# Optimization experiments

Measured on AMD Instinct MI355X. Metric: run time of the kernel, lower is better.

The kernel has to match this reference:

```python
import jax, jax.numpy as jnp
import numpy as np

WS = (7, 7)   # window size
SS = (3, 3)   # shift size
NH = 3        # num heads
EPS = 1e-5


def _rel_index():
    # relative position index [N, N], computed exactly as in WindowAttention.__init__
    coords = np.stack(np.meshgrid(np.arange(WS[0]), np.arange(WS[1]), indexing='ij'))  # [2,7,7]
    cf = coords.reshape(2, -1)                     # [2, N]
    rel = (cf[:, :, None] - cf[:, None, :]).transpose(1, 2, 0)  # [N, N, 2]
    rel[..., 0] += WS[0] - 1
    rel[..., 1] += WS[1] - 1
    idx = rel[..., 0] * (2 * WS[1] - 1) + rel[..., 1]
    return jnp.asarray(idx)


def _attn_mask(H, W):
    # standard Swin shifted-window mask: [nW, N, N] of {0, -100}
    img = np.zeros((H, W), dtype=np.float32)
    cnt = 0
    for hs in (slice(0, -WS[0]), slice(-WS[0], -SS[0]), slice(-SS[0], None)):
        for ws_ in (slice(0, -WS[1]), slice(-WS[1], -SS[1]), slice(-SS[1], None)):
            img[hs, ws_] = cnt
            cnt += 1
    mw = img.reshape(H // WS[0], WS[0], W // WS[1], WS[1]).transpose(0, 2, 1, 3)
    mw = mw.reshape(-1, WS[0] * WS[1])            # [nW, N]
    am = mw[:, None, :] - mw[:, :, None]
    am = np.where(am != 0, np.float32(-100.0), np.float32(0.0))
    return jnp.asarray(am)


def _ln(x, g, b):
    m = x.mean(-1, keepdims=True)
    v = ((x - m) ** 2).mean(-1, keepdims=True)
    return (x - m) * jax.lax.rsqrt(v + EPS) * g + b


def _forward(x, norm1_g, norm1_b, qkv_w, qkv_b, rel_table, proj_w, proj_b,
             norm2_g, norm2_b, mlp_w1, mlp_b1, mlp_w2, mlp_b2):
    B, C, H, W = x.shape
    N = WS[0] * WS[1]
    hd = C // NH
    scale = hd ** -0.5

    # norm1 over channels (token layout [B, HW, C])
    xt = x.reshape(B, C, H * W).transpose(0, 2, 1)
    xn = _ln(xt, norm1_g, norm1_b).transpose(0, 2, 1).reshape(B, C, H, W)

    # cyclic shift + window partition -> [B*nW, N, C]
    shifted = jnp.roll(xn, (-SS[0], -SS[1]), axis=(2, 3))
    nWh, nWw = H // WS[0], W // WS[1]
    xw = shifted.transpose(0, 2, 3, 1)  # [B, H, W, C]
    xwin = xw.reshape(B, nWh, WS[0], nWw, WS[1], C).transpose(0, 1, 3, 2, 4, 5)
    xwin = xwin.reshape(-1, N, C)

    # windowed attention with relative position bias + shift mask
    qkv = (xwin @ qkv_w.T + qkv_b).reshape(-1, N, 3, NH, hd).transpose(2, 0, 3, 1, 4)
    q, k, v = qkv[0] * scale, qkv[1], qkv[2]            # [B_, h, N, hd]
    attn = jnp.einsum('bhnd,bhmd->bhnm', q, k)          # [B_, h, N, N]
    bias = rel_table[_rel_index()]                       # [N, N, h]
    attn = attn + bias.transpose(2, 0, 1)[None]
    mask = _attn_mask(H, W)                              # [nW, N, N]
    nW = mask.shape[0]
    attn = attn.reshape(-1, nW, NH, N, N) + mask[None, :, None]
    attn = jax.nn.softmax(attn.reshape(-1, NH, N, N), axis=-1)
    out = jnp.einsum('bhnm,bhmd->bhnd', attn, v).transpose(0, 2, 1, 3).reshape(-1, N, C)
    out = out @ proj_w.T + proj_b

    # window reverse + reverse shift -> [B, C, H, W]
    xr = out.reshape(B, nWh, nWw, WS[0], WS[1], C).transpose(0, 1, 3, 2, 4, 5)
    xr = xr.reshape(B, H, W, C).transpose(0, 3, 1, 2)
    xr = jnp.roll(xr, (SS[0], SS[1]), axis=(2, 3))

    x = x + xr  # residual (drop_path = Identity)

    # MLP branch with pre-norm over channels
    xt = x.reshape(B, C, H * W).transpose(0, 2, 1)
    h = _ln(xt, norm2_g, norm2_b)
    h = jax.nn.gelu(h @ mlp_w1.T + mlp_b1, approximate=False)
    h = h @ mlp_w2.T + mlp_b2
    return x + h.transpose(0, 2, 1).reshape(B, C, H, W)


def setup_inputs() -> dict:
    key = jax.random.key(0)
    ks = jax.random.split(key, 8)
    B, C, H, W = 8, 96, 224, 224
    hid = 384
    s = 0.02
    return {
        'x': jax.random.normal(ks[0], (B, C, H, W), jnp.float32),
        'norm1_g': jnp.ones((C,), jnp.float32),
        'norm1_b': jnp.zeros((C,), jnp.float32),
        'qkv_w': jax.random.normal(ks[1], (3 * C, C), jnp.float32) * s,
        'qkv_b': jnp.zeros((3 * C,), jnp.float32),
        'rel_table': jax.random.normal(ks[2], (169, NH), jnp.float32) * s,
        'proj_w': jax.random.normal(ks[3], (C, C), jnp.float32) * s,
        'proj_b': jnp.zeros((C,), jnp.float32),
        'norm2_g': jnp.ones((C,), jnp.float32),
        'norm2_b': jnp.zeros((C,), jnp.float32),
        'mlp_w1': jax.random.normal(ks[4], (hid, C), jnp.float32) * s,
        'mlp_b1': jnp.zeros((hid,), jnp.float32),
        'mlp_w2': jax.random.normal(ks[5], (C, hid), jnp.float32) * s,
        'mlp_b2': jnp.zeros((C,), jnp.float32),
    }


def reference(x, norm1_g, norm1_b, qkv_w, qkv_b, rel_table, proj_w, proj_b,
              norm2_g, norm2_b, mlp_w1, mlp_b1, mlp_w2, mlp_b2):
    return _forward(x, norm1_g, norm1_b, qkv_w, qkv_b, rel_table, proj_w, proj_b,
                    norm2_g, norm2_b, mlp_w1, mlp_b1, mlp_w2, mlp_b2)
```

## Files before the change

### kernel.cpp

```cpp
#include <hip/hip_runtime.h>
#include <hip/hip_bf16.h>

typedef __attribute__((ext_vector_type(8))) short short8;
typedef __attribute__((ext_vector_type(4))) short s16x4;
typedef __attribute__((ext_vector_type(4))) float f32x4;

#define D_H   224
#define D_W   224
#define D_HW  50176
#define SCALE 0.17677669529663687f

#define WO_QKVW  0
#define WO_PROJW 27648
#define WO_W1    36864
#define WO_W2    73728
#define WO_TOT   110592

#define XT_SH 0
#define YT_SH 38535168
#define W_SH  77070336
#define TAB_SH (W_SH + WO_TOT)
#define WS_NEED ((size_t)(77070336 + 110592) * 2 + 65536)

static __device__ __forceinline__ short f2s(float v) {
    union { __hip_bfloat16 b; short s; } u; u.b = __float2bfloat16(v); return u.s;
}
static __device__ __forceinline__ float s2f(short s) {
    union { short s; __hip_bfloat16 b; } u; u.s = s; return __bfloat162float(u.b);
}

#define MFMA(a, b, c) __builtin_amdgcn_mfma_f32_16x16x32_bf16((a), (b), (c), 0, 0, 0)

static __device__ __forceinline__ short8 normfrag(const short* p, const float* g,
                                                  const float* b, int c0, float m, float rs) {
    short8 r = *(const short8*)p;
    short8 o;
#pragma unroll
    for (int j = 0; j < 8; j++) o[j] = f2s((s2f(r[j]) - m) * rs * g[c0 + j] + b[c0 + j]);
    return o;
}

static __device__ __forceinline__ float erf_fast(float x) {
    float a = fabsf(x);
    float t = __builtin_amdgcn_rcpf(1.f + 0.3275911f * a);
    float p = t * (0.254829592f + t * (-0.284496736f + t * (1.421413741f +
              t * (-1.453152027f + t * 1.061405429f))));
    float y = 1.f - p * __expf(-a * a);
    return copysignf(y, x);
}

__global__ __launch_bounds__(256) void k_prep(
    const float* __restrict__ qkvw, const float* __restrict__ projw,
    const float* __restrict__ w1, const float* __restrict__ w2,
    const float* __restrict__ relt, short* __restrict__ ws, float* __restrict__ tabf)
{
    const int bid = blockIdx.x;
    if (bid < 108) {
        int i4 = bid * 256 + threadIdx.x;
        const float* src; int off;
        if (i4 < 6912)        { src = qkvw;  off = 0; }
        else if (i4 < 9216)   { src = projw; off = 6912; }
        else if (i4 < 18432)  { src = w1;    off = 9216; }
        else                  { src = w2;    off = 18432; }
        f32x4 v = *(const f32x4*)&src[(i4 - off) * 4];
        s16x4 s;
#pragma unroll
        for (int j = 0; j < 4; j++) s[j] = f2s(v[j]);
        *(s16x4*)&ws[i4 * 4] = s;
    } else {
        int i = (bid - 108) * 256 + threadIdx.x;
        int n = i >> 6, m = i & 63;
        int nn = (n < 49) ? n : 48;
        int mm = (m < 49) ? m : 48;
        int r1 = nn / 7, c1 = nn - r1 * 7;
        int r2 = mm / 7, c2 = mm - r2 * 7;
        int ri = ((r1 - r2 + 6) * 13 + (c1 - c2 + 6)) * 3;
        f32x4 o = { relt[ri + 0], relt[ri + 1], relt[ri + 2], 0.f };
        *(f32x4*)&tabf[i * 4] = o;
    }
}

__global__ __launch_bounds__(256) void k_t(const float* __restrict__ x, short* __restrict__ xt)
{
    __shared__ short tile[224][128];
    const int tid = threadIdx.x;
    const int bh = blockIdx.x;
    const int b = bh / 224, h = bh - b * 224;
    const int pbase = (b * 96) * D_HW + h * 224;

#pragma unroll
    for (int k = 0; k < 6; k++) {
        int idx = tid + k * 256;
        if (idx < 1344) {
            int c4 = idx / 56, w4 = idx - c4 * 56;
            float vv[4][4];
#pragma unroll
            for (int j = 0; j < 4; j++) {
                f32x4 v = *(const f32x4*)&x[pbase + (c4 * 4 + j) * D_HW + w4 * 4];
#pragma unroll
                for (int i = 0; i < 4; i++) vv[j][i] = v[i];
            }
#pragma unroll
            for (int i = 0; i < 4; i++) {
                int w = w4 * 4 + i;
                s16x4 o;
#pragma unroll
                for (int j = 0; j < 4; j++) o[j] = f2s(vv[j][i]);
                *(s16x4*)&tile[w][(c4 ^ (w & 31)) * 4] = o;
            }
        }
    }
    __syncthreads();
    const int obase = ((b * 224 + h) * 224) * 96;
#pragma unroll
    for (int k = 0; k < 11; k++) {
        int idx = tid + k * 256;
        if (idx < 2688) {
            int w = idx / 12, s = idx - w * 12;
            int kk = w & 31;
            s16x4 a = *(const s16x4*)&tile[w][((2 * s) ^ kk) * 4];
            s16x4 c = *(const s16x4*)&tile[w][((2 * s + 1) ^ kk) * 4];
            short8 o;
            o[0] = a[0]; o[1] = a[1]; o[2] = a[2]; o[3] = a[3];
            o[4] = c[0]; o[5] = c[1]; o[6] = c[2]; o[7] = c[3];
            *(short8*)&xt[obase + w * 96 + s * 8] = o;
        }
    }
}

__global__ __launch_bounds__(256, 3) void k_attn_t(
    const short* __restrict__ xt, const float* __restrict__ n1g, const float* __restrict__ n1b,
    const float* __restrict__ qkvb, const float* __restrict__ tabf,
    const float* __restrict__ projb, const short* __restrict__ wsw, short* __restrict__ yt)
{
    __shared__ short qk[64][200];
    __shared__ __align__(16) short region[11520];
    short (*xs)[104] = (short(*)[104])region;
    short (*ps)[72]  = (short(*)[72])region;
    short (*vt)[72]  = (short(*)[72])(region + 4608);
    __shared__ int   cnt_s[64];
    __shared__ float mean_s[64], rstd_s[64];

    const int tid  = threadIdx.x;
    const int wave = tid >> 6, lane = tid & 63;
    const int l16  = lane & 15, q8 = (lane >> 4) * 8, q4 = (lane >> 4) * 4;
    const int t0   = wave * 16;

    const short* qkvw_bf  = wsw + WO_QKVW;
    const short* projw_bf = wsw + WO_PROJW;

    const int wi = blockIdx.x;
    const int b  = wi >> 10, nw = wi & 1023;
    const int wh = nw >> 5, ww = nw & 31;
    const bool edge = (wh == 31) || (ww == 31);

    if (tid < 64) {
        int t = (tid < 49) ? tid : 48;
        int r = t / 7, c = t - r * 7;
        int sh = wh * 7 + r, sw = ww * 7 + c;
        int rh = (sh < 217) ? 0 : ((sh < 221) ? 1 : 2);
        int rw = (sw < 217) ? 0 : ((sw < 221) ? 1 : 2);
        cnt_s[tid] = rh * 3 + rw;
    }
#pragma unroll
    for (int k = 0; k < 3; k++) {
        int idx = tid + k * 256;
        int t = idx / 12, s = idx - t * 12;
        short8 v = {0, 0, 0, 0, 0, 0, 0, 0};
        if (t < 49) {
            int r = t / 7, cc = t - r * 7;
            int hh = wh * 7 + r + 3;  if (hh >= D_H) hh -= D_H;
            int w2 = ww * 7 + cc + 3; if (w2 >= D_W) w2 -= D_W;
            v = *(const short8*)&xt[((b * 224 + hh) * 224 + w2) * 96 + s * 8];
        }
        *(short8*)&xs[t][s * 8] = v;
    }
    __syncthreads();

    {
        int t = tid >> 2, p = tid & 3;
        float s = 0.f, s2 = 0.f;
#pragma unroll
        for (int i = 0; i < 6; i++) {
            s16x4 v4 = *(const s16x4*)&xs[t][p * 24 + i * 4];
#pragma unroll
            for (int j = 0; j < 4; j++) { float v = s2f(v4[j]); s += v; s2 += v * v; }
        }
        s += __shfl_xor(s, 1); s2 += __shfl_xor(s2, 1);
        s += __shfl_xor(s, 2); s2 += __shfl_xor(s2, 2);
        if (p == 0) {
            float m = s * (1.f / 96.f);
            float var = s2 * (1.f / 96.f) - m * m;
            mean_s[t] = m; rstd_s[t] = rsqrtf(var + 1e-5f);
        }
    }

    const float m0 = mean_s[t0 + l16], rs0 = rstd_s[t0 + l16];
    short8 a0 = normfrag(&xs[t0 + l16][q8],      n1g, n1b, q8,      m0, rs0);
    short8 a1 = normfrag(&xs[t0 + l16][32 + q8], n1g, n1b, 32 + q8, m0, rs0);
    short8 a2 = normfrag(&xs[t0 + l16][64 + q8], n1g, n1b, 64 + q8, m0, rs0);

    short8 wA0, wA1, wA2, wB0, wB1, wB2;
    {
        const short* w = qkvw_bf + l16 * 96;
        wA0 = *(const short8*)&w[q8];
        wA1 = *(const short8*)&w[32 + q8];
        wA2 = *(const short8*)&w[64 + q8];
    }
    __syncthreads();

#pragma unroll
    for (int g = 0; g < 18; g++) {
        const int jc = g / 6, nt = g - jc * 6;
        const int jj = nt * 16 + l16;
        if (g < 17) {
            int g2 = g + 1, jc2 = g2 / 6, nt2 = g2 - jc2 * 6;
            const short* w = qkvw_bf + (jc2 * 96 + nt2 * 16 + l16) * 96;
            wB0 = *(const short8*)&w[q8];
            wB1 = *(const short8*)&w[32 + q8];
            wB2 = *(const short8*)&w[64 + q8];
        }
        f32x4 acc = {0.f, 0.f, 0.f, 0.f};
        acc = MFMA(a0, wA0, acc);
        acc = MFMA(a1, wA1, acc);
        acc = MFMA(a2, wA2, acc);
        float bias = qkvb[jc * 96 + jj];
        if (jc == 0) {
#pragma unroll
            for (int r = 0; r < 4; r++) qk[t0 + q4 + r][jj] = f2s((acc[r] + bias) * SCALE);
        } else if (jc == 1) {
#pragma unroll
            for (int r = 0; r < 4; r++) qk[t0 + q4 + r][96 + jj] = f2s(acc[r] + bias);
        } else {
            s16x4 v4;
#pragma unroll
            for (int r = 0; r < 4; r++) v4[r] = f2s(acc[r] + bias);
            *(s16x4*)&vt[jj][t0 + q4] = v4;
        }
        wA0 = wB0; wA1 = wB1; wA2 = wB2;
    }

    float biasv[4][4][3];
#pragma unroll
    for (int nt = 0; nt < 4; nt++) {
        int m  = nt * 16 + l16;
        int cm = cnt_s[m];
#pragma unroll
        for (int r = 0; r < 4; r++) {
            int n = t0 + q4 + r;
            f32x4 t4 = *(const f32x4*)&tabf[(n * 64 + m) * 4];
            float mk = (edge && (cnt_s[n] != cm)) ? -100.f : 0.f;
            biasv[nt][r][0] = t4[0] + mk;
            biasv[nt][r][1] = t4[1] + mk;
            biasv[nt][r][2] = t4[2] + mk;
        }
    }
    const bool inval3 = (l16 != 0);

    __syncthreads();

#pragma unroll
    for (int h = 0; h < 3; h++) {
        short8 aq = *(const short8*)&qk[t0 + l16][h * 32 + q8];
        f32x4 sv[4];
#pragma unroll
        for (int nt = 0; nt < 4; nt++) {
            f32x4 z = {0.f, 0.f, 0.f, 0.f};
            sv[nt] = MFMA(aq, *(const short8*)&qk[nt * 16 + l16][96 + h * 32 + q8], z);
        }
        float mx[4] = {-1e30f, -1e30f, -1e30f, -1e30f};
#pragma unroll
        for (int nt = 0; nt < 4; nt++) {
#pragma unroll
            for (int r = 0; r < 4; r++) {
                float v = sv[nt][r] + biasv[nt][r][h];
                if (nt == 3 && inval3) v = -1e30f;
                sv[nt][r] = v;
                mx[r] = fmaxf(mx[r], v);
            }
        }
#pragma unroll
        for (int d = 1; d < 16; d <<= 1) {
#pragma unroll
            for (int r = 0; r < 4; r++) mx[r] = fmaxf(mx[r], __shfl_xor(mx[r], d));
        }
        float sm[4] = {0.f, 0.f, 0.f, 0.f};
#pragma unroll
        for (int nt = 0; nt < 4; nt++) {
#pragma unroll
            for (int r = 0; r < 4; r++) {
                float e = (nt == 3 && inval3) ? 0.f : __expf(sv[nt][r] - mx[r]);
                sv[nt][r] = e;
                sm[r] += e;
            }
        }
#pragma unroll
        for (int d = 1; d < 16; d <<= 1) {
#pragma unroll
            for (int r = 0; r < 4; r++) sm[r] += __shfl_xor(sm[r], d);
        }
        float inv[4];
#pragma unroll
        for (int r = 0; r < 4; r++) inv[r] = __builtin_amdgcn_rcpf(sm[r]);
#pragma unroll
        for (int nt = 0; nt < 4; nt++) {
#pragma unroll
            for (int r = 0; r < 4; r++)
                ps[t0 + q4 + r][nt * 16 + l16] = f2s(sv[nt][r] * inv[r]);
        }
        short8 p0 = *(const short8*)&ps[t0 + l16][q8];
        short8 p1 = *(const short8*)&ps[t0 + l16][32 + q8];
#pragma unroll
        for (int nt = 0; nt < 2; nt++) {
            f32x4 acc = {0.f, 0.f, 0.f, 0.f};
            acc = MFMA(p0, *(const short8*)&vt[h * 32 + nt * 16 + l16][q8],      acc);
            acc = MFMA(p1, *(const short8*)&vt[h * 32 + nt * 16 + l16][32 + q8], acc);
            int d = nt * 16 + l16;
#pragma unroll
            for (int r = 0; r < 4; r++) {
                int t = t0 + q4 + r;
                if (t < 49) qk[t][h * 32 + d] = f2s(acc[r]);
            }
        }
    }

    {
        const short* w = projw_bf + l16 * 96;
        wA0 = *(const short8*)&w[q8];
        wA1 = *(const short8*)&w[32 + q8];
        wA2 = *(const short8*)&w[64 + q8];
    }
    short8 o0 = *(const short8*)&qk[t0 + l16][q8];
    short8 o1 = *(const short8*)&qk[t0 + l16][32 + q8];
    short8 o2 = *(const short8*)&qk[t0 + l16][64 + q8];
#pragma unroll
    for (int nt = 0; nt < 6; nt++) {
        int i = nt * 16 + l16;
        if (nt < 5) {
            const short* w = projw_bf + ((nt + 1) * 16 + l16) * 96;
            wB0 = *(const short8*)&w[q8];
            wB1 = *(const short8*)&w[32 + q8];
            wB2 = *(const short8*)&w[64 + q8];
        }
        f32x4 acc = {0.f, 0.f, 0.f, 0.f};
        acc = MFMA(o0, wA0, acc);
        acc = MFMA(o1, wA1, acc);
        acc = MFMA(o2, wA2, acc);
        float pb = projb[i];
#pragma unroll
        for (int r = 0; r < 4; r++) {
            int t = t0 + q4 + r;
            if (t < 49) qk[t][i] = f2s(acc[r] + pb);
        }
        wA0 = wB0; wA1 = wB1; wA2 = wB2;
    }
    __syncthreads();
#pragma unroll
    for (int k = 0; k < 3; k++) {
        int idx = tid + k * 256;
        if (idx < 588) {
            int t = idx / 12, s = idx - t * 12;
            int r = t / 7, cc = t - r * 7;
            int hh = wh * 7 + r + 3;  if (hh >= D_H) hh -= D_H;
            int w2 = ww * 7 + cc + 3; if (w2 >= D_W) w2 -= D_W;
            *(short8*)&yt[((b * 224 + hh) * 224 + w2) * 96 + s * 8] =
                *(const short8*)&qk[t][s * 8];
        }
    }
}

#define XCOL(row, c) ((((((c) >> 3) ^ (((row) >> 2) & 7)) << 3)) | ((c) & 7))

__global__ __launch_bounds__(256, 3) void k_mlp_t(
    const float* __restrict__ x, const short* __restrict__ ytk, float* __restrict__ y,
    const float* __restrict__ n2g, const float* __restrict__ n2b,
    const float* __restrict__ b1, const float* __restrict__ b2, const short* __restrict__ wsw)
{
    __shared__ __align__(16) char region[96 * 104 * 2];
    short (*xs)[128] = (short(*)[128])region;
    short (*wb)[104] = (short(*)[104])region;
    __shared__ __align__(16) short hb[64][104];
    __shared__ float mean_s[64], rstd_s[64];

    const int tid  = threadIdx.x;
    const int wave = tid >> 6, lane = tid & 63;
    const int l16  = lane & 15, q8 = (lane >> 4) * 8, q4 = (lane >> 4) * 4;
    const int t0   = wave * 16;

    const short* w1_bf = wsw + WO_W1;
    const short* w2_bf = wsw + WO_W2;

    const int T0 = blockIdx.x * 64;
    const int b  = T0 / D_HW;
    const int p0 = T0 - b * D_HW;
    const int base = (b * 96) * D_HW + p0;

#pragma unroll
    for (int k = 0; k < 3; k++) {
        int idx = tid + k * 256;
        int t = idx / 12, s = idx - t * 12;
        *(short8*)&xs[t][(s ^ ((t >> 2) & 7)) << 3] =
            *(const short8*)&ytk[(T0 + t) * 96 + s * 8];
    }
    __syncthreads();

    float yv[6][4];
#pragma unroll
    for (int k = 0; k < 6; k++) {
        int idx = tid + k * 256;
        int c = idx >> 4, q = idx & 15;
        f32x4 xv = *(const f32x4*)&x[base + c * D_HW + q * 4];
        int ch = ((c >> 3) ^ (q & 7)) * 8 + (c & 7);
#pragma unroll
        for (int j = 0; j < 4; j++) {
            float v = xv[j] + s2f(xs[q * 4 + j][ch]);
            yv[k][j] = v;
            xs[q * 4 + j][ch] = f2s(v);
        }
    }
    __syncthreads();

    {
        int t = tid >> 2, p = tid & 3;
        float s = 0.f, s2 = 0.f;
#pragma unroll
        for (int i = 0; i < 6; i++) {
            int c = p * 24 + i * 4;
            s16x4 v4 = *(const s16x4*)&xs[t][XCOL(t, c)];
#pragma unroll
            for (int j = 0; j < 4; j++) { float v = s2f(v4[j]); s += v; s2 += v * v; }
        }
        s += __shfl_xor(s, 1); s2 += __shfl_xor(s2, 1);
        s += __shfl_xor(s, 2); s2 += __shfl_xor(s2, 2);
        if (p == 0) {
            float m = s * (1.f / 96.f);
            float var = s2 * (1.f / 96.f) - m * m;
            mean_s[t] = m; rstd_s[t] = rsqrtf(var + 1e-5f);
        }
    }

    short8 xa[3];
    {
        int t = t0 + l16;
        float m = mean_s[t], rs = rstd_s[t];
        int key = (t >> 2) & 7;
#pragma unroll
        for (int kk = 0; kk < 3; kk++) {
            int ch = kk * 4 + (lane >> 4);
            xa[kk] = normfrag(&xs[t][(ch ^ key) << 3], n2g, n2b, ch * 8, m, rs);
        }
    }

    f32x4 c2[6];
#pragma unroll
    for (int nt = 0; nt < 6; nt++) c2[nt] = (f32x4){0.f, 0.f, 0.f, 0.f};

    short8 pf[5];
#pragma unroll
    for (int k = 0; k < 5; k++) {
        int idx = tid + k * 256; if (idx > 1151) idx = 1151;
        pf[k] = *(const short8*)&w1_bf[idx * 8];
    }
#pragma unroll
    for (int jc = 0; jc < 4; jc++) {
        __syncthreads();
#pragma unroll
        for (int k = 0; k < 5; k++) {
            int idx = tid + k * 256;
            if (idx < 1152) { int j = idx / 12, s = idx - j * 12; *(short8*)&wb[j][s * 8] = pf[k]; }
        }
        __syncthreads();
#pragma unroll
        for (int k = 0; k < 5; k++) {
            int idx = tid + k * 256; if (idx > 1151) idx = 1151;
            int o = idx / 12, s = idx - o * 12;
            pf[k] = *(const short8*)&w2_bf[o * 384 + jc * 96 + s * 8];
        }
#pragma unroll
        for (int nt = 0; nt < 6; nt++) {
            int jj = nt * 16 + l16;
            f32x4 acc = {0.f, 0.f, 0.f, 0.f};
            acc = MFMA(xa[0], *(const short8*)&wb[jj][q8],      acc);
            acc = MFMA(xa[1], *(const short8*)&wb[jj][32 + q8], acc);
            acc = MFMA(xa[2], *(const short8*)&wb[jj][64 + q8], acc);
            float bb = b1[jc * 96 + jj];
#pragma unroll
            for (int r = 0; r < 4; r++) {
                float v = acc[r] + bb;
                float g = 0.5f * v * (1.f + erf_fast(v * 0.7071067811865475f));
                hb[t0 + q4 + r][jj] = f2s(g);
            }
        }
        __syncthreads();
#pragma unroll
        for (int k = 0; k < 5; k++) {
            int idx = tid + k * 256;
            if (idx < 1152) { int j = idx / 12, s = idx - j * 12; *(short8*)&wb[j][s * 8] = pf[k]; }
        }
        __syncthreads();
        if (jc < 3) {
#pragma unroll
            for (int k = 0; k < 5; k++) {
                int idx = tid + k * 256; if (idx > 1151) idx = 1151;
                pf[k] = *(const short8*)&w1_bf[(jc + 1) * 9216 + idx * 8];
            }
        }
        {
            short8 h0 = *(const short8*)&hb[t0 + l16][q8];
            short8 h1 = *(const short8*)&hb[t0 + l16][32 + q8];
            short8 h2 = *(const short8*)&hb[t0 + l16][64 + q8];
#pragma unroll
            for (int nt = 0; nt < 6; nt++) {
                int jj = nt * 16 + l16;
                c2[nt] = MFMA(h0, *(const short8*)&wb[jj][q8],      c2[nt]);
                c2[nt] = MFMA(h1, *(const short8*)&wb[jj][32 + q8], c2[nt]);
                c2[nt] = MFMA(h2, *(const short8*)&wb[jj][64 + q8], c2[nt]);
            }
        }
    }
    __syncthreads();

#pragma unroll
    for (int nt = 0; nt < 6; nt++) {
        int i = nt * 16 + l16;
        float bo = b2[i];
#pragma unroll
        for (int r = 0; r < 4; r++) {
            int t = t0 + q4 + r;
            xs[t][XCOL(t, i)] = f2s(bo + c2[nt][r]);
        }
    }
    __syncthreads();
#pragma unroll
    for (int k = 0; k < 6; k++) {
        int idx = tid + k * 256;
        int c = idx >> 4, q = idx & 15;
        int ch = ((c >> 3) ^ (q & 7)) * 8 + (c & 7);
        f32x4 o;
#pragma unroll
        for (int j = 0; j < 4; j++) o[j] = yv[k][j] + s2f(xs[q * 4 + j][ch]);
        *(f32x4*)&y[base + c * D_HW + q * 4] = o;
    }
}

__global__ __launch_bounds__(256, 3) void k_attn_f(
    const float* __restrict__ x, const float* __restrict__ n1g, const float* __restrict__ n1b,
    const float* __restrict__ qkvb, const float* __restrict__ relt,
    const float* __restrict__ projb, const short* __restrict__ wsw, float* __restrict__ y)
{
    __shared__ short qk[64][200];
    __shared__ short vt[96][72];
    __shared__ __align__(16) short xs[64][104];
    short (*ps)[72] = (short(*)[72])xs;
    __shared__ int   cnt_s[64];
    __shared__ float mean_s[64], rstd_s[64];

    const int tid  = threadIdx.x;
    const int wave = tid >> 6, lane = tid & 63;
    const int l16  = lane & 15, q8 = (lane >> 4) * 8, q4 = (lane >> 4) * 4;
    const int t0   = wave * 16;

    const short* qkvw_bf  = wsw + WO_QKVW;
    const short* projw_bf = wsw + WO_PROJW;

    const int wi = blockIdx.x;
    const int b  = wi >> 10, nw = wi & 1023;
    const int wh = nw >> 5, ww = nw & 31;
    const bool edge = (wh == 31) || (ww == 31);

    if (tid < 64) {
        int t = (tid < 49) ? tid : 48;
        int r = t / 7, c = t - r * 7;
        int sh = wh * 7 + r, sw = ww * 7 + c;
        int rh = (sh < 217) ? 0 : ((sh < 221) ? 1 : 2);
        int rw = (sw < 217) ? 0 : ((sw < 221) ? 1 : 2);
        cnt_s[tid] = rh * 3 + rw;
    }
    {
        int t = lane;
        int r = t / 7, cc = t - r * 7;
        int hh = wh * 7 + r + 3;  if (hh >= D_H) hh -= D_H;
        int w2 = ww * 7 + cc + 3; if (w2 >= D_W) w2 -= D_W;
        int off0 = (b * 96) * D_HW + hh * D_W + w2;
#pragma unroll
        for (int n = 0; n < 6; n++) {
            int c0 = wave * 24 + n * 4;
            s16x4 v4 = {0, 0, 0, 0};
            if (t < 49) {
                v4[0] = f2s(x[off0 + (c0 + 0) * D_HW]);
                v4[1] = f2s(x[off0 + (c0 + 1) * D_HW]);
                v4[2] = f2s(x[off0 + (c0 + 2) * D_HW]);
                v4[3] = f2s(x[off0 + (c0 + 3) * D_HW]);
            }
            *(s16x4*)&xs[t][c0] = v4;
        }
    }
    __syncthreads();
    {
        int t = tid >> 2, p = tid & 3;
        float s = 0.f, s2 = 0.f;
#pragma unroll
        for (int i = 0; i < 6; i++) {
            s16x4 v4 = *(const s16x4*)&xs[t][p * 24 + i * 4];
#pragma unroll
            for (int j = 0; j < 4; j++) { float v = s2f(v4[j]); s += v; s2 += v * v; }
        }
        s += __shfl_xor(s, 1); s2 += __shfl_xor(s2, 1);
        s += __shfl_xor(s, 2); s2 += __shfl_xor(s2, 2);
        if (p == 0) {
            float m = s * (1.f / 96.f);
            float var = s2 * (1.f / 96.f) - m * m;
            mean_s[t] = m; rstd_s[t] = rsqrtf(var + 1e-5f);
        }
    }
    __syncthreads();

    const float m0 = mean_s[t0 + l16], rs0 = rstd_s[t0 + l16];
    short8 a0 = normfrag(&xs[t0 + l16][q8],      n1g, n1b, q8,      m0, rs0);
    short8 a1 = normfrag(&xs[t0 + l16][32 + q8], n1g, n1b, 32 + q8, m0, rs0);
    short8 a2 = normfrag(&xs[t0 + l16][64 + q8], n1g, n1b, 64 + q8, m0, rs0);

#pragma unroll
    for (int jc = 0; jc < 3; jc++) {
#pragma unroll
        for (int nt = 0; nt < 6; nt++) {
            int jj = nt * 16 + l16;
            const short* wr = qkvw_bf + (jc * 96 + jj) * 96;
            f32x4 acc = {0.f, 0.f, 0.f, 0.f};
            acc = MFMA(a0, *(const short8*)&wr[q8],      acc);
            acc = MFMA(a1, *(const short8*)&wr[32 + q8], acc);
            acc = MFMA(a2, *(const short8*)&wr[64 + q8], acc);
            float bias = qkvb[jc * 96 + jj];
            if (jc == 0) {
#pragma unroll
                for (int r = 0; r < 4; r++) qk[t0 + q4 + r][jj] = f2s((acc[r] + bias) * SCALE);
            } else if (jc == 1) {
#pragma unroll
                for (int r = 0; r < 4; r++) qk[t0 + q4 + r][96 + jj] = f2s(acc[r] + bias);
            } else {
                s16x4 v4;
#pragma unroll
                for (int r = 0; r < 4; r++) v4[r] = f2s(acc[r] + bias);
                *(s16x4*)&vt[jj][t0 + q4] = v4;
            }
        }
    }

    float biasv[4][4][3];
#pragma unroll
    for (int nt = 0; nt < 4; nt++) {
        int m  = nt * 16 + l16;
        int mm = (m < 49) ? m : 48;
        int r2 = mm / 7, c2 = mm - r2 * 7;
        int cm = cnt_s[m];
#pragma unroll
        for (int r = 0; r < 4; r++) {
            int n  = t0 + q4 + r;
            int nn = (n < 49) ? n : 48;
            int r1 = nn / 7, c1 = nn - r1 * 7;
            int ri = ((r1 - r2 + 6) * 13 + (c1 - c2 + 6)) * 3;
            float mk = (edge && (cnt_s[n] != cm)) ? -100.f : 0.f;
            biasv[nt][r][0] = relt[ri + 0] + mk;
            biasv[nt][r][1] = relt[ri + 1] + mk;
            biasv[nt][r][2] = relt[ri + 2] + mk;
        }
    }
    const bool inval3 = (l16 != 0);

#pragma unroll
    for (int h = 0; h < 3; h++) {
        __syncthreads();
        short8 aq = *(const short8*)&qk[t0 + l16][h * 32 + q8];
        f32x4 sv[4];
#pragma unroll
        for (int nt = 0; nt < 4; nt++) {
            f32x4 z = {0.f, 0.f, 0.f, 0.f};
            sv[nt] = MFMA(aq, *(const short8*)&qk[nt * 16 + l16][96 + h * 32 + q8], z);
        }
        float mx[4] = {-1e30f, -1e30f, -1e30f, -1e30f};
#pragma unroll
        for (int nt = 0; nt < 4; nt++) {
#pragma unroll
            for (int r = 0; r < 4; r++) {
                float v = sv[nt][r] + biasv[nt][r][h];
                if (nt == 3 && inval3) v = -1e30f;
                sv[nt][r] = v;
                mx[r] = fmaxf(mx[r], v);
            }
        }
#pragma unroll
        for (int d = 1; d < 16; d <<= 1) {
#pragma unroll
            for (int r = 0; r < 4; r++) mx[r] = fmaxf(mx[r], __shfl_xor(mx[r], d));
        }
        float sm[4] = {0.f, 0.f, 0.f, 0.f};
#pragma unroll
        for (int nt = 0; nt < 4; nt++) {
#pragma unroll
            for (int r = 0; r < 4; r++) {
                float e = (nt == 3 && inval3) ? 0.f : __expf(sv[nt][r] - mx[r]);
                sv[nt][r] = e;
                sm[r] += e;
            }
        }
#pragma unroll
        for (int d = 1; d < 16; d <<= 1) {
#pragma unroll
            for (int r = 0; r < 4; r++) sm[r] += __shfl_xor(sm[r], d);
        }
        float inv[4];
#pragma unroll
        for (int r = 0; r < 4; r++) inv[r] = 1.f / sm[r];
#pragma unroll
        for (int nt = 0; nt < 4; nt++) {
#pragma unroll
            for (int r = 0; r < 4; r++)
                ps[t0 + q4 + r][nt * 16 + l16] = f2s(sv[nt][r] * inv[r]);
        }
        __syncthreads();
        short8 p0 = *(const short8*)&ps[t0 + l16][q8];
        short8 p1 = *(const short8*)&ps[t0 + l16][32 + q8];
#pragma unroll
        for (int nt = 0; nt < 2; nt++) {
            f32x4 acc = {0.f, 0.f, 0.f, 0.f};
            acc = MFMA(p0, *(const short8*)&vt[h * 32 + nt * 16 + l16][q8],      acc);
            acc = MFMA(p1, *(const short8*)&vt[h * 32 + nt * 16 + l16][32 + q8], acc);
            int d = nt * 16 + l16;
#pragma unroll
            for (int r = 0; r < 4; r++) {
                int t = t0 + q4 + r;
                if (t < 49) qk[t][h * 32 + d] = f2s(acc[r]);
            }
        }
    }

    __syncthreads();
    short8 o0 = *(const short8*)&qk[t0 + l16][q8];
    short8 o1 = *(const short8*)&qk[t0 + l16][32 + q8];
    short8 o2 = *(const short8*)&qk[t0 + l16][64 + q8];
    int  po[4];
    bool tv[4];
#pragma unroll
    for (int r = 0; r < 4; r++) {
        int t = t0 + q4 + r;
        tv[r] = (t < 49);
        int tt = tv[r] ? t : 0;
        int rr = tt / 7, cc = tt - rr * 7;
        int hh = wh * 7 + rr + 3;  if (hh >= D_H) hh -= D_H;
        int w2 = ww * 7 + cc + 3;  if (w2 >= D_W) w2 -= D_W;
        po[r] = (b * 96) * D_HW + hh * D_W + w2;
    }
#pragma unroll
    for (int nt = 0; nt < 6; nt++) {
        int i = nt * 16 + l16;
        const short* wr = projw_bf + i * 96;
        f32x4 acc = {0.f, 0.f, 0.f, 0.f};
        acc = MFMA(o0, *(const short8*)&wr[q8],      acc);
        acc = MFMA(o1, *(const short8*)&wr[32 + q8], acc);
        acc = MFMA(o2, *(const short8*)&wr[64 + q8], acc);
        float pb = projb[i];
#pragma unroll
        for (int r = 0; r < 4; r++) {
            if (tv[r]) {
                int off = po[r] + i * D_HW;
                y[off] = x[off] + acc[r] + pb;
            }
        }
    }
}

__global__ __launch_bounds__(256, 3) void k_mlp_f(
    float* __restrict__ y, const float* __restrict__ n2g, const float* __restrict__ n2b,
    const float* __restrict__ b1, const float* __restrict__ b2, const short* __restrict__ wsw)
{
    __shared__ short xs[128][104];
    __shared__ short hb[128][104];
    __shared__ float mean_s[128], rstd_s[128];

    const int tid  = threadIdx.x;
    const int wave = tid >> 6, lane = tid & 63;
    const int l16  = lane & 15, q8 = (lane >> 4) * 8, q4 = (lane >> 4) * 4;
    const int t0   = wave * 32;

    const short* w1_bf = wsw + WO_W1;
    const short* w2_bf = wsw + WO_W2;

    const int T0 = blockIdx.x * 128;
    const int b  = T0 / D_HW;
    const int p0 = T0 - b * D_HW;
    const int base = (b * 96) * D_HW + p0;

    for (int idx = tid; idx < 96 * 32; idx += 256) {
        int c = idx >> 5, q = idx & 31;
        f32x4 v4 = *(const f32x4*)&y[base + c * D_HW + q * 4];
        xs[q * 4 + 0][c] = f2s(v4[0]);
        xs[q * 4 + 1][c] = f2s(v4[1]);
        xs[q * 4 + 2][c] = f2s(v4[2]);
        xs[q * 4 + 3][c] = f2s(v4[3]);
    }
    __syncthreads();
    {
        int t = tid >> 1, p = tid & 1;
        float s = 0.f, s2 = 0.f;
#pragma unroll
        for (int i = 0; i < 12; i++) {
            s16x4 v4 = *(const s16x4*)&xs[t][p * 48 + i * 4];
#pragma unroll
            for (int j = 0; j < 4; j++) { float v = s2f(v4[j]); s += v; s2 += v * v; }
        }
        s += __shfl_xor(s, 1); s2 += __shfl_xor(s2, 1);
        float m = s * (1.f / 96.f);
        float var = s2 * (1.f / 96.f) - m * m;
        mean_s[t] = m; rstd_s[t] = rsqrtf(var + 1e-5f);
    }
    __syncthreads();

    short8 xa[2][3];
#pragma unroll
    for (int s = 0; s < 2; s++) {
        float m = mean_s[t0 + s * 16 + l16], rs = rstd_s[t0 + s * 16 + l16];
#pragma unroll
        for (int kk = 0; kk < 3; kk++)
            xa[s][kk] = normfrag(&xs[t0 + s * 16 + l16][kk * 32 + q8], n2g, n2b,
                                 kk * 32 + q8, m, rs);
    }

    f32x4 c2[2][6];
#pragma unroll
    for (int s = 0; s < 2; s++)
#pragma unroll
        for (int nt = 0; nt < 6; nt++) c2[s][nt] = (f32x4){0.f, 0.f, 0.f, 0.f};

    for (int jc = 0; jc < 4; jc++) {
#pragma unroll
        for (int s = 0; s < 2; s++) {
#pragma unroll
            for (int nt = 0; nt < 6; nt++) {
                int jj = nt * 16 + l16;
                const short* wr = w1_bf + (jc * 96 + jj) * 96;
                f32x4 acc = {0.f, 0.f, 0.f, 0.f};
                acc = MFMA(xa[s][0], *(const short8*)&wr[q8],      acc);
                acc = MFMA(xa[s][1], *(const short8*)&wr[32 + q8], acc);
                acc = MFMA(xa[s][2], *(const short8*)&wr[64 + q8], acc);
                float bb = b1[jc * 96 + jj];
#pragma unroll
                for (int r = 0; r < 4; r++) {
                    float v = acc[r] + bb;
                    float g = 0.5f * v * (1.f + erf_fast(v * 0.7071067811865475f));
                    hb[t0 + s * 16 + q4 + r][jj] = f2s(g);
                }
            }
        }
        __syncthreads();
#pragma unroll
        for (int s = 0; s < 2; s++) {
            short8 h0 = *(const short8*)&hb[t0 + s * 16 + l16][q8];
            short8 h1 = *(const short8*)&hb[t0 + s * 16 + l16][32 + q8];
            short8 h2 = *(const short8*)&hb[t0 + s * 16 + l16][64 + q8];
#pragma unroll
            for (int nt = 0; nt < 6; nt++) {
                const short* wr = w2_bf + (nt * 16 + l16) * 384 + jc * 96;
                c2[s][nt] = MFMA(h0, *(const short8*)&wr[q8],      c2[s][nt]);
                c2[s][nt] = MFMA(h1, *(const short8*)&wr[32 + q8], c2[s][nt]);
                c2[s][nt] = MFMA(h2, *(const short8*)&wr[64 + q8], c2[s][nt]);
            }
        }
        __syncthreads();
    }

#pragma unroll
    for (int s = 0; s < 2; s++)
#pragma unroll
        for (int nt = 0; nt < 6; nt++) {
            int i = nt * 16 + l16;
            float bo = b2[i];
#pragma unroll
            for (int r = 0; r < 4; r++)
                xs[t0 + s * 16 + q4 + r][i] = f2s(bo + c2[s][nt][r]);
        }
    __syncthreads();
    for (int idx = tid; idx < 96 * 32; idx += 256) {
        int c = idx >> 5, q = idx & 31;
        int off = base + c * D_HW + q * 4;
        f32x4 v4 = *(const f32x4*)&y[off];
        v4[0] += s2f(xs[q * 4 + 0][c]);
        v4[1] += s2f(xs[q * 4 + 1][c]);
        v4[2] += s2f(xs[q * 4 + 2][c]);
        v4[3] += s2f(xs[q * 4 + 3][c]);
        *(f32x4*)&y[off] = v4;
    }
}

extern "C" void kernel_launch(void* const* d_in, const int* in_sizes, int n_in,
                              void* d_out, int out_size, void* d_ws, size_t ws_size,
                              hipStream_t stream) {
    const float* x    = (const float*)d_in[0];
    const float* n1g  = (const float*)d_in[1];
    const float* n1b  = (const float*)d_in[2];
    const float* qkvw = (const float*)d_in[3];
    const float* qkvb = (const float*)d_in[4];
    const float* relt = (const float*)d_in[5];
    const float* projw= (const float*)d_in[6];
    const float* projb= (const float*)d_in[7];
    const float* n2g  = (const float*)d_in[8];
    const float* n2b  = (const float*)d_in[9];
    const float* w1   = (const float*)d_in[10];
    const float* b1   = (const float*)d_in[11];
    const float* w2   = (const float*)d_in[12];
    const float* b2   = (const float*)d_in[13];
    float* y  = (float*)d_out;
    short* ws = (short*)d_ws;

    if (ws_size >= WS_NEED) {
        short* xt  = ws + XT_SH;
        short* ytk = ws + YT_SH;
        short* wbf = ws + W_SH;
        float* tabf = (float*)(ws + TAB_SH);
        k_prep<<<124, 256, 0, stream>>>(qkvw, projw, w1, w2, relt, wbf, tabf);
        k_t<<<1792, 256, 0, stream>>>(x, xt);
        k_attn_t<<<8192, 256, 0, stream>>>(xt, n1g, n1b, qkvb, tabf, projb, wbf, ytk);
        k_mlp_t<<<6272, 256, 0, stream>>>(x, ytk, y, n2g, n2b, b1, b2, wbf);
    } else {
        k_prep<<<108, 256, 0, stream>>>(qkvw, projw, w1, w2, relt, ws, (float*)ws);
        k_attn_f<<<8192, 256, 0, stream>>>(x, n1g, n1b, qkvb, relt, projb, ws, y);
        k_mlp_f<<<3136, 256, 0, stream>>>(y, n2g, n2b, b1, b2, ws);
    }
}
```

Measured before the change: 676.9 us.

## Move LayerNorm1 into transpose kernel and compute rel-pos bias inline

LayerNorm1 statistics and normalization move from the attention kernel into the transpose kernel, so the stored bf16 token tensor is already normalized and the attention kernel loads its A fragments directly. The precomputed relative-position bias table is dropped, and the attention kernel gathers bias values straight from the small rel_table with index arithmetic. This removes per-window LN work and the table build/load, but adds an extra LN pass in the transpose kernel and scattered small loads in attention.

Measured after the change: 632.0 us. 6.6% less time.

```diff
diff --git a/kernel.cpp b/kernel.cpp
--- a/kernel.cpp
+++ b/kernel.cpp
@@ -19,8 +19,7 @@
 #define XT_SH 0
 #define YT_SH 38535168
 #define W_SH  77070336
-#define TAB_SH (W_SH + WO_TOT)
-#define WS_NEED ((size_t)(77070336 + 110592) * 2 + 65536)
+#define WS_NEED ((size_t)(77070336 + 110592) * 2)
 
 static __device__ __forceinline__ short f2s(float v) {
     union { __hip_bfloat16 b; short s; } u; u.b = __float2bfloat16(v); return u.s;
@@ -51,38 +50,27 @@
 
 __global__ __launch_bounds__(256) void k_prep(
     const float* __restrict__ qkvw, const float* __restrict__ projw,
-    const float* __restrict__ w1, const float* __restrict__ w2,
-    const float* __restrict__ relt, short* __restrict__ ws, float* __restrict__ tabf)
+    const float* __restrict__ w1, const float* __restrict__ w2, short* __restrict__ ws)
 {
-    const int bid = blockIdx.x;
-    if (bid < 108) {
-        int i4 = bid * 256 + threadIdx.x;
-        const float* src; int off;
-        if (i4 < 6912)        { src = qkvw;  off = 0; }
-        else if (i4 < 9216)   { src = projw; off = 6912; }
-        else if (i4 < 18432)  { src = w1;    off = 9216; }
-        else                  { src = w2;    off = 18432; }
-        f32x4 v = *(const f32x4*)&src[(i4 - off) * 4];
-        s16x4 s;
-#pragma unroll
-        for (int j = 0; j < 4; j++) s[j] = f2s(v[j]);
-        *(s16x4*)&ws[i4 * 4] = s;
-    } else {
-        int i = (bid - 108) * 256 + threadIdx.x;
-        int n = i >> 6, m = i & 63;
-        int nn = (n < 49) ? n : 48;
-        int mm = (m < 49) ? m : 48;
-        int r1 = nn / 7, c1 = nn - r1 * 7;
-        int r2 = mm / 7, c2 = mm - r2 * 7;
-        int ri = ((r1 - r2 + 6) * 13 + (c1 - c2 + 6)) * 3;
-        f32x4 o = { relt[ri + 0], relt[ri + 1], relt[ri + 2], 0.f };
-        *(f32x4*)&tabf[i * 4] = o;
-    }
-}
-
-__global__ __launch_bounds__(256) void k_t(const float* __restrict__ x, short* __restrict__ xt)
+    int i4 = blockIdx.x * 256 + threadIdx.x;
+    const float* src; int off;
+    if (i4 < 6912)        { src = qkvw;  off = 0; }
+    else if (i4 < 9216)   { src = projw; off = 6912; }
+    else if (i4 < 18432)  { src = w1;    off = 9216; }
+    else                  { src = w2;    off = 18432; }
+    f32x4 v = *(const f32x4*)&src[(i4 - off) * 4];
+    s16x4 s;
+#pragma unroll
+    for (int j = 0; j < 4; j++) s[j] = f2s(v[j]);
+    *(s16x4*)&ws[i4 * 4] = s;
+}
+
+__global__ __launch_bounds__(256) void k_t(
+    const float* __restrict__ x, const float* __restrict__ n1g,
+    const float* __restrict__ n1b, short* __restrict__ xt)
 {
     __shared__ short tile[224][128];
+    __shared__ float mean_s[224], rstd_s[224];
     const int tid = threadIdx.x;
     const int bh = blockIdx.x;
     const int b = bh / 224, h = bh - b * 224;
@@ -111,6 +99,20 @@
         }
     }
     __syncthreads();
+    if (tid < 224) {
+        int key = tid & 31;
+        float s = 0.f, s2 = 0.f;
+#pragma unroll
+        for (int c4 = 0; c4 < 24; c4++) {
+            s16x4 v4 = *(const s16x4*)&tile[tid][(c4 ^ key) << 2];
+#pragma unroll
+            for (int j = 0; j < 4; j++) { float v = s2f(v4[j]); s += v; s2 += v * v; }
+        }
+        float m = s * (1.f / 96.f);
+        float var = s2 * (1.f / 96.f) - m * m;
+        mean_s[tid] = m; rstd_s[tid] = rsqrtf(var + 1e-5f);
+    }
+    __syncthreads();
     const int obase = ((b * 224 + h) * 224) * 96;
 #pragma unroll
     for (int k = 0; k < 11; k++) {
@@ -118,20 +120,27 @@
         if (idx < 2688) {
             int w = idx / 12, s = idx - w * 12;
             int kk = w & 31;
-            s16x4 a = *(const s16x4*)&tile[w][((2 * s) ^ kk) * 4];
-            s16x4 c = *(const s16x4*)&tile[w][((2 * s + 1) ^ kk) * 4];
+            s16x4 a = *(const s16x4*)&tile[w][((2 * s) ^ kk) << 2];
+            s16x4 c = *(const s16x4*)&tile[w][((2 * s + 1) ^ kk) << 2];
+            float m = mean_s[w], rs = rstd_s[w];
+            f32x4 g0 = *(const f32x4*)&n1g[s * 8];
+            f32x4 g1 = *(const f32x4*)&n1g[s * 8 + 4];
+            f32x4 b0 = *(const f32x4*)&n1b[s * 8];
+            f32x4 b1 = *(const f32x4*)&n1b[s * 8 + 4];
             short8 o;
-            o[0] = a[0]; o[1] = a[1]; o[2] = a[2]; o[3] = a[3];
-            o[4] = c[0]; o[5] = c[1]; o[6] = c[2]; o[7] = c[3];
+#pragma unroll
+            for (int j = 0; j < 4; j++) o[j]     = f2s((s2f(a[j]) - m) * rs * g0[j] + b0[j]);
+#pragma unroll
+            for (int j = 0; j < 4; j++) o[4 + j] = f2s((s2f(c[j]) - m) * rs * g1[j] + b1[j]);
             *(short8*)&xt[obase + w * 96 + s * 8] = o;
         }
     }
 }
 
 __global__ __launch_bounds__(256, 3) void k_attn_t(
-    const short* __restrict__ xt, const float* __restrict__ n1g, const float* __restrict__ n1b,
-    const float* __restrict__ qkvb, const float* __restrict__ tabf,
-    const float* __restrict__ projb, const short* __restrict__ wsw, short* __restrict__ yt)
+    const short* __restrict__ xt, const float* __restrict__ qkvb,
+    const float* __restrict__ relt, const float* __restrict__ projb,
+    const short* __restrict__ wsw, short* __restrict__ yt)
 {
     __shared__ short qk[64][200];
     __shared__ __align__(16) short region[11520];
@@ -139,7 +148,6 @@
     short (*ps)[72]  = (short(*)[72])region;
     short (*vt)[72]  = (short(*)[72])(region + 4608);
     __shared__ int   cnt_s[64];
-    __shared__ float mean_s[64], rstd_s[64];
 
     const int tid  = threadIdx.x;
     const int wave = tid >> 6, lane = tid & 63;
@@ -177,28 +185,9 @@
     }
     __syncthreads();
 
-    {
-        int t = tid >> 2, p = tid & 3;
-        float s = 0.f, s2 = 0.f;
-#pragma unroll
-        for (int i = 0; i < 6; i++) {
-            s16x4 v4 = *(const s16x4*)&xs[t][p * 24 + i * 4];
-#pragma unroll
-            for (int j = 0; j < 4; j++) { float v = s2f(v4[j]); s += v; s2 += v * v; }
-        }
-        s += __shfl_xor(s, 1); s2 += __shfl_xor(s2, 1);
-        s += __shfl_xor(s, 2); s2 += __shfl_xor(s2, 2);
-        if (p == 0) {
-            float m = s * (1.f / 96.f);
-            float var = s2 * (1.f / 96.f) - m * m;
-            mean_s[t] = m; rstd_s[t] = rsqrtf(var + 1e-5f);
-        }
-    }
-
-    const float m0 = mean_s[t0 + l16], rs0 = rstd_s[t0 + l16];
-    short8 a0 = normfrag(&xs[t0 + l16][q8],      n1g, n1b, q8,      m0, rs0);
-    short8 a1 = normfrag(&xs[t0 + l16][32 + q8], n1g, n1b, 32 + q8, m0, rs0);
-    short8 a2 = normfrag(&xs[t0 + l16][64 + q8], n1g, n1b, 64 + q8, m0, rs0);
+    short8 a0 = *(const short8*)&xs[t0 + l16][q8];
+    short8 a1 = *(const short8*)&xs[t0 + l16][32 + q8];
+    short8 a2 = *(const short8*)&xs[t0 + l16][64 + q8];
 
     short8 wA0, wA1, wA2, wB0, wB1, wB2;
     {
@@ -244,15 +233,19 @@
 #pragma unroll
     for (int nt = 0; nt < 4; nt++) {
         int m  = nt * 16 + l16;
+        int mm = (m < 49) ? m : 48;
+        int r2 = mm / 7, c2 = mm - r2 * 7;
         int cm = cnt_s[m];
 #pragma unroll
         for (int r = 0; r < 4; r++) {
-            int n = t0 + q4 + r;
-            f32x4 t4 = *(const f32x4*)&tabf[(n * 64 + m) * 4];
+            int n  = t0 + q4 + r;
+            int nn = (n < 49) ? n : 48;
+            int r1 = nn / 7, c1 = nn - r1 * 7;
+            int ri = ((r1 - r2 + 6) * 13 + (c1 - c2 + 6)) * 3;
             float mk = (edge && (cnt_s[n] != cm)) ? -100.f : 0.f;
-            biasv[nt][r][0] = t4[0] + mk;
-            biasv[nt][r][1] = t4[1] + mk;
-            biasv[nt][r][2] = t4[2] + mk;
+            biasv[nt][r][0] = relt[ri + 0] + mk;
+            biasv[nt][r][1] = relt[ri + 1] + mk;
+            biasv[nt][r][2] = relt[ri + 2] + mk;
         }
     }
     const bool inval3 = (l16 != 0);
@@ -915,13 +908,12 @@
         short* xt  = ws + XT_SH;
         short* ytk = ws + YT_SH;
         short* wbf = ws + W_SH;
-        float* tabf = (float*)(ws + TAB_SH);
-        k_prep<<<124, 256, 0, stream>>>(qkvw, projw, w1, w2, relt, wbf, tabf);
-        k_t<<<1792, 256, 0, stream>>>(x, xt);
-        k_attn_t<<<8192, 256, 0, stream>>>(xt, n1g, n1b, qkvb, tabf, projb, wbf, ytk);
+        k_prep<<<108, 256, 0, stream>>>(qkvw, projw, w1, w2, wbf);
+        k_t<<<1792, 256, 0, stream>>>(x, n1g, n1b, xt);
+        k_attn_t<<<8192, 256, 0, stream>>>(xt, qkvb, relt, projb, wbf, ytk);
         k_mlp_t<<<6272, 256, 0, stream>>>(x, ytk, y, n2g, n2b, b1, b2, wbf);
     } else {
-        k_prep<<<108, 256, 0, stream>>>(qkvw, projw, w1, w2, relt, ws, (float*)ws);
+        k_prep<<<108, 256, 0, stream>>>(qkvw, projw, w1, w2, ws);
         k_attn_f<<<8192, 256, 0, stream>>>(x, n1g, n1b, qkvb, relt, projb, ws, y);
         k_mlp_f<<<3136, 256, 0, stream>>>(y, n2g, n2b, b1, b2, ws);
     }
```
